# Kernel optimization log

Measured on AMD Instinct MI355X. Metric: run time of the kernel, lower is better.

The kernel has to match this reference:

```python
import jax, jax.numpy as jnp
import numpy as np
import math

D_MODEL = 1024
N_HEADS = 16
D_K = D_MODEL // N_HEADS
SEQ_LEN = 2048
BATCH = 2


def setup_inputs() -> dict:
    key = jax.random.key(0)
    ks = jax.random.split(key, 5)
    X = jax.random.normal(ks[0], (BATCH, SEQ_LEN, D_MODEL), dtype=jnp.float32)
    # Linear params (torch Linear: y = x @ W.T + b). Store as [in, out] for einsum.
    sc1 = 1.0 / math.sqrt(D_MODEL)
    W_qkv = jax.random.uniform(ks[1], (D_MODEL, 3 * D_MODEL), jnp.float32, -sc1, sc1)
    b_qkv = jax.random.uniform(ks[2], (3 * D_MODEL,), jnp.float32, -sc1, sc1)
    W_out = jax.random.uniform(ks[3], (D_MODEL, D_MODEL), jnp.float32, -sc1, sc1)
    b_out = jax.random.uniform(ks[4], (D_MODEL,), jnp.float32, -sc1, sc1)
    return {"X": X, "W_qkv": W_qkv, "b_qkv": b_qkv, "W_out": W_out, "b_out": b_out}


def reference(X, W_qkv, b_qkv, W_out, b_out):
    B, S, E = X.shape
    qkv = X @ W_qkv + b_qkv                       # [B,S,3E]
    qkv = qkv.reshape(B, S, 3, N_HEADS, D_K)
    q = jnp.transpose(qkv[:, :, 0], (0, 2, 1, 3))  # [B,H,S,Dk]
    k = jnp.transpose(qkv[:, :, 1], (0, 2, 1, 3))
    v = jnp.transpose(qkv[:, :, 2], (0, 2, 1, 3))
    scores = jnp.einsum('bhqd,bhkd->bhqk', q, k) / math.sqrt(D_K)
    causal = jnp.tril(jnp.ones((S, S), dtype=bool))
    scores = jnp.where(causal[None, None], scores, -jnp.inf)
    probs = jax.nn.softmax(scores, axis=-1)
    out = jnp.einsum('bhqk,bhkd->bhqd', probs, v)  # [B,H,S,Dk]
    out = jnp.transpose(out, (0, 2, 1, 3)).reshape(B, S, E)
    return out @ W_out + b_out
```

## Files before the change

### kernel.cpp

```cpp
#include <hip/hip_runtime.h>

typedef __bf16 bf16_t;
typedef bf16_t bf16x8 __attribute__((ext_vector_type(8)));
typedef bf16_t bf16x4 __attribute__((ext_vector_type(4)));
typedef float f32x4 __attribute__((ext_vector_type(4)));

#define SEQLEN 2048
#define EMB 1024
#define NHEADS 16
#define N3 3072
#define NBATCH 2
#define NEG_INF (-__builtin_inff())
#define SC2 0.18033688011112042f

__device__ __forceinline__ void async16(bf16_t* lds, const bf16_t* g) {
    __builtin_amdgcn_global_load_lds(
        (const __attribute__((address_space(1))) void*)g,
        (__attribute__((address_space(3))) void*)lds, 16, 0, 0);
}

__global__ __launch_bounds__(256) void transpose_weights(
    const float* __restrict__ Wqkv, const float* __restrict__ Wout,
    bf16_t* __restrict__ Wqkv_t, bf16_t* __restrict__ Wout_t)
{
    __shared__ float tile[64][65];
    int bx = blockIdx.x;
    const int k0 = blockIdx.y * 64;
    const float* W; bf16_t* Wt; int N; float s;
    if (bx < 48) { W = Wqkv; Wt = Wqkv_t; N = N3;  s = (bx * 64 < EMB) ? SC2 : 1.0f; }
    else         { bx -= 48; W = Wout; Wt = Wout_t; N = EMB; s = 1.0f; }
    const int n0 = bx * 64;
    const int t = threadIdx.x;
    const int nl = t & 63, k4 = t >> 6;
#pragma unroll
    for (int i = 0; i < 16; ++i) {
        int kk = k4 + i * 4;
        tile[kk][nl] = W[(size_t)(k0 + kk) * N + n0 + nl];
    }
    __syncthreads();
    const int kl = t & 63, n4 = t >> 6;
#pragma unroll
    for (int i = 0; i < 16; ++i) {
        int nn = n4 + i * 4;
        Wt[(size_t)(n0 + nn) * EMB + k0 + kl] = (bf16_t)(tile[kl][nn] * s);
    }
}

__global__ __launch_bounds__(256) void cvt_f32_bf16(
    const float* __restrict__ in, bf16_t* __restrict__ out, int n)
{
    const int i = (blockIdx.x * 256 + threadIdx.x) * 8;
    if (i >= n) return;
    float4 a = *(const float4*)&in[i];
    float4 b = *(const float4*)&in[i + 4];
    bf16_t v[8];
    v[0] = (bf16_t)a.x; v[1] = (bf16_t)a.y; v[2] = (bf16_t)a.z; v[3] = (bf16_t)a.w;
    v[4] = (bf16_t)b.x; v[5] = (bf16_t)b.y; v[6] = (bf16_t)b.z; v[7] = (bf16_t)b.w;
    *(float4*)&out[i] = *(float4*)&v[0];
}

template<bool OUT_BF16, bool V_SPLIT>
__global__ __launch_bounds__(256) void gemm_bt_kernel(
    const bf16_t* __restrict__ A, const bf16_t* __restrict__ Bt,
    const float* __restrict__ bias, void* __restrict__ Cp,
    bf16_t* __restrict__ vt, int scale_q,
    int Mdim, int Ndim, int Kdim)
{
    __shared__ bf16_t As[128 * 64];
    __shared__ bf16_t Bs[128 * 64];
    const int nb = Ndim >> 7;
    const int cpx = gridDim.x >> 3;
    const int bid = (blockIdx.x & 7) * cpx + (blockIdx.x >> 3);
    const int bx = bid % nb, by = bid / nb;
    const int r0 = by << 7, c0 = bx << 7;
    const int t = threadIdx.x, lane = t & 63;
    const int wid = t >> 6;
    const int wm = wid >> 1, wn = wid & 1;
    const int lr = lane & 15, lg = lane >> 4;

    const int glrow = wid * 32 + (lane >> 3);
    const int gsw = ((lane & 7) ^ (lane >> 3)) << 3;
    const bf16_t* gA = &A[(size_t)(r0 + glrow) * Kdim + gsw];
    const bf16_t* gB = &Bt[(size_t)(c0 + glrow) * Kdim + gsw];
    bf16_t* ldsA = &As[wid * 2048];
    bf16_t* ldsB = &Bs[wid * 2048];
    const size_t row8 = (size_t)8 * Kdim;

    const int fragb0 = (lr * 128 + lg * 16) ^ ((lr & 7) << 4);
    const int fragb1 = (lr * 128 + 64 + lg * 16) ^ ((lr & 7) << 4);

    f32x4 acc[4][4] = {};
    const int KT = Kdim >> 6;
    for (int kt = 0; kt < KT; ++kt) {
        const bf16_t* a = gA + kt * 64;
        const bf16_t* b = gB + kt * 64;
        async16(ldsA,        a);
        async16(ldsA + 512,  a + row8);
        async16(ldsA + 1024, a + 2 * row8);
        async16(ldsA + 1536, a + 3 * row8);
        async16(ldsB,        b);
        async16(ldsB + 512,  b + row8);
        async16(ldsB + 1024, b + 2 * row8);
        async16(ldsB + 1536, b + 3 * row8);
        __syncthreads();

        const char* Ab = (const char*)As + wm * 8192;
        const char* Bb = (const char*)Bs + wn * 8192;
        bf16x8 af[4], bfm[4];
#pragma unroll
        for (int m = 0; m < 4; ++m)
            af[m] = *(const bf16x8*)(Ab + m * 2048 + fragb0);
#pragma unroll
        for (int n = 0; n < 4; ++n)
            bfm[n] = *(const bf16x8*)(Bb + n * 2048 + fragb0);
#pragma unroll
        for (int m = 0; m < 4; ++m)
#pragma unroll
            for (int n = 0; n < 4; ++n)
                acc[m][n] = __builtin_amdgcn_mfma_f32_16x16x32_bf16(
                    af[m], bfm[n], acc[m][n], 0, 0, 0);
#pragma unroll
        for (int m = 0; m < 4; ++m)
            af[m] = *(const bf16x8*)(Ab + m * 2048 + fragb1);
#pragma unroll
        for (int n = 0; n < 4; ++n)
            bfm[n] = *(const bf16x8*)(Bb + n * 2048 + fragb1);
#pragma unroll
        for (int m = 0; m < 4; ++m)
#pragma unroll
            for (int n = 0; n < 4; ++n)
                acc[m][n] = __builtin_amdgcn_mfma_f32_16x16x32_bf16(
                    af[m], bfm[n], acc[m][n], 0, 0, 0);
        __syncthreads();
    }

    const bool vmode = V_SPLIT && (c0 >= 2 * EMB);
#pragma unroll
    for (int m = 0; m < 4; ++m) {
#pragma unroll
        for (int n = 0; n < 4; ++n) {
            const int col = c0 + wn * 64 + n * 16 + lr;
            float bval = bias[col];
            if (scale_q && col < EMB) bval *= SC2;
            if (vmode) {
                const int h = (col - 2 * EMB) >> 6, dd = col & 63;
                const int bb = r0 >> 11;
                const int sbase = (r0 & (SEQLEN - 1)) + wm * 64 + m * 16 + lg * 4;
                bf16x4 pk;
#pragma unroll
                for (int j = 0; j < 4; ++j) pk[j] = (bf16_t)(acc[m][n][j] + bval);
                *(bf16x4*)&vt[(size_t)((bb * 16 + h) * 64 + dd) * SEQLEN + sbase] = pk;
            } else {
#pragma unroll
                for (int j = 0; j < 4; ++j) {
                    const int row = r0 + wm * 64 + m * 16 + lg * 4 + j;
                    const float v = acc[m][n][j] + bval;
                    if (OUT_BF16)
                        ((bf16_t*)Cp)[(size_t)row * Ndim + col] = (bf16_t)v;
                    else
                        ((float*)Cp)[(size_t)row * Ndim + col] = v;
                }
            }
        }
    }
}

__global__ __launch_bounds__(256, 4) void attn_kernel(
    const bf16_t* __restrict__ qkv, const bf16_t* __restrict__ vt,
    bf16_t* __restrict__ attn_out)
{
    __shared__ bf16_t Kl[2][4096];
    __shared__ bf16_t Vl[2][4096];
    const int d = blockIdx.x;
    const int r = d >> 8;
    const int u = (d >> 3) & 31;
    int qt = (r & 1) ? (31 - u) : u;
    if (r & 2) qt ^= 16;
    const int bh = (d & 7) + (r << 3);
    const int b = bh >> 4, h = bh & 15;
    const int q0 = qt << 6;
    const int t = threadIdx.x, lane = t & 63, wid = t >> 6;
    const int lr = lane & 15, lg = lane >> 4;
    const int sr = t >> 2, sc16 = (t & 3) << 4;

    const int fragb0 = (lr * 128 + lg * 16) ^ ((lr & 7) << 4);
    const int fragb1 = (lr * 128 + 64 + lg * 16) ^ ((lr & 7) << 4);
    const int stb0   = (sr * 128 + sc16 * 2) ^ ((sr & 7) << 4);
    const int stb1   = (sr * 128 + sc16 * 2 + 16) ^ ((sr & 7) << 4);

    const bf16_t* kp = &qkv[(size_t)(b * SEQLEN + sr) * N3 + EMB + h * 64 + sc16];
    const bf16_t* vp = &vt[(size_t)(bh * 64 + sr) * SEQLEN + sc16];
    const size_t kstep = (size_t)64 * N3;

    const int qg = q0 + wid * 16 + lr;
    bf16x8 qa0, qa1;
    {
        const bf16_t* qb = &qkv[(size_t)(b * SEQLEN + qg) * N3 + h * 64];
        qa0 = *(const bf16x8*)&qb[lg * 8];
        qa1 = *(const bf16x8*)&qb[32 + lg * 8];
    }
    bf16x8 ones;
#pragma unroll
    for (int i = 0; i < 8; ++i) ones[i] = (bf16_t)1.0f;

    f32x4 o[4] = {};
    f32x4 ol = {};
    float m_run = NEG_INF;

    auto stK = [&](char* base, float4 a, float4 c) {
        *(float4*)(base + stb0) = a; *(float4*)(base + stb1) = c;
    };
    auto stV = [&](char* base, float4 a, float4 c) {
        float4 w0 = {a.x, a.y, c.x, c.y};
        float4 w1 = {a.z, a.w, c.z, c.w};
        *(float4*)(base + stb0) = w0; *(float4*)(base + stb1) = w1;
    };

    {
        float4 k0 = *(const float4*)kp, k1 = *(const float4*)(kp + 8);
        float4 v0 = *(const float4*)vp, v1 = *(const float4*)(vp + 8);
        stK((char*)Kl[0], k0, k1);
        stV((char*)Vl[0], v0, v1);
    }
    __syncthreads();
    int cur = 0;
    for (int kt = 0; kt <= qt; ++kt) {
        float4 nk0, nk1, nv0, nv1;
        const bool more = (kt < qt);
        if (more) {
            kp += kstep; vp += 64;
            nk0 = *(const float4*)kp; nk1 = *(const float4*)(kp + 8);
            nv0 = *(const float4*)vp; nv1 = *(const float4*)(vp + 8);
        }

        const char* Kc = (const char*)Kl[cur];
        const char* Vc = (const char*)Vl[cur];

        f32x4 sc[4] = {};
        __builtin_amdgcn_s_setprio(1);
#pragma unroll
        for (int n = 0; n < 4; ++n) {
            bf16x8 kb0 = *(const bf16x8*)(Kc + (fragb0 + n * 2048));
            bf16x8 kb1 = *(const bf16x8*)(Kc + (fragb1 + n * 2048));
            sc[n] = __builtin_amdgcn_mfma_f32_16x16x32_bf16(kb0, qa0, sc[n], 0, 0, 0);
            sc[n] = __builtin_amdgcn_mfma_f32_16x16x32_bf16(kb1, qa1, sc[n], 0, 0, 0);
        }
        __builtin_amdgcn_s_setprio(0);

        if (kt == qt) {
#pragma unroll
            for (int n = 0; n < 4; ++n)
#pragma unroll
                for (int j = 0; j < 4; ++j) {
                    const int kg = kt * 64 + n * 16 + lg * 4 + j;
                    sc[n][j] = (kg <= qg) ? sc[n][j] : NEG_INF;
                }
        }
        float mx[4];
#pragma unroll
        for (int n = 0; n < 4; ++n)
            mx[n] = fmaxf(fmaxf(fmaxf(sc[n][0], sc[n][1]), sc[n][2]), sc[n][3]);
        float pmax = fmaxf(fmaxf(fmaxf(mx[0], mx[1]), mx[2]), mx[3]);

        if (__any(pmax > m_run + 8.f)) {
            float pm = fmaxf(pmax, __shfl_xor(pmax, 16));
            pm = fmaxf(pm, __shfl_xor(pm, 32));
            const float mnew = fmaxf(m_run, pm);
            const float alpha = exp2f(m_run - mnew);
            m_run = mnew;
            float al[4];
#pragma unroll
            for (int j = 0; j < 4; ++j) al[j] = __shfl(alpha, lg * 4 + j);
#pragma unroll
            for (int dn = 0; dn < 4; ++dn)
#pragma unroll
                for (int j = 0; j < 4; ++j) o[dn][j] *= al[j];
#pragma unroll
            for (int j = 0; j < 4; ++j) ol[j] *= al[j];
        }

#pragma unroll
        for (int n = 0; n < 4; ++n)
#pragma unroll
            for (int j = 0; j < 4; ++j) sc[n][j] = exp2f(sc[n][j] - m_run);

        unsigned pk00, pk01, pk10, pk11, pk20, pk21, pk30, pk31;
        asm("v_cvt_pk_bf16_f32 %0, %1, %2" : "=v"(pk00) : "v"(sc[0][0]), "v"(sc[0][1]));
        asm("v_cvt_pk_bf16_f32 %0, %1, %2" : "=v"(pk01) : "v"(sc[0][2]), "v"(sc[0][3]));
        asm("v_cvt_pk_bf16_f32 %0, %1, %2" : "=v"(pk10) : "v"(sc[1][0]), "v"(sc[1][1]));
        asm("v_cvt_pk_bf16_f32 %0, %1, %2" : "=v"(pk11) : "v"(sc[1][2]), "v"(sc[1][3]));
        asm("v_cvt_pk_bf16_f32 %0, %1, %2" : "=v"(pk20) : "v"(sc[2][0]), "v"(sc[2][1]));
        asm("v_cvt_pk_bf16_f32 %0, %1, %2" : "=v"(pk21) : "v"(sc[2][2]), "v"(sc[2][3]));
        asm("v_cvt_pk_bf16_f32 %0, %1, %2" : "=v"(pk30) : "v"(sc[3][0]), "v"(sc[3][1]));
        asm("v_cvt_pk_bf16_f32 %0, %1, %2" : "=v"(pk31) : "v"(sc[3][2]), "v"(sc[3][3]));
        asm("v_permlane32_swap_b32 %0, %1" : "+v"(pk00), "+v"(pk10));
        asm("v_permlane32_swap_b32 %0, %1" : "+v"(pk01), "+v"(pk11));
        asm("v_permlane32_swap_b32 %0, %1" : "+v"(pk20), "+v"(pk30));
        asm("v_permlane32_swap_b32 %0, %1" : "+v"(pk21), "+v"(pk31));
        union UW { unsigned w[4]; bf16x8 v; };
        UW ua, ub;
        ua.w[0] = pk00; ua.w[1] = pk01; ua.w[2] = pk10; ua.w[3] = pk11;
        ub.w[0] = pk20; ub.w[1] = pk21; ub.w[2] = pk30; ub.w[3] = pk31;
        const bf16x8 pa0 = ua.v, pa1 = ub.v;

        __builtin_amdgcn_s_setprio(1);
#pragma unroll
        for (int dn = 0; dn < 4; ++dn) {
            bf16x8 vb0 = *(const bf16x8*)(Vc + (fragb0 + dn * 2048));
            bf16x8 vb1 = *(const bf16x8*)(Vc + (fragb1 + dn * 2048));
            o[dn] = __builtin_amdgcn_mfma_f32_16x16x32_bf16(pa0, vb0, o[dn], 0, 0, 0);
            o[dn] = __builtin_amdgcn_mfma_f32_16x16x32_bf16(pa1, vb1, o[dn], 0, 0, 0);
        }
        ol = __builtin_amdgcn_mfma_f32_16x16x32_bf16(pa0, ones, ol, 0, 0, 0);
        ol = __builtin_amdgcn_mfma_f32_16x16x32_bf16(pa1, ones, ol, 0, 0, 0);
        __builtin_amdgcn_s_setprio(0);

        if (more) {
            stK((char*)Kl[cur ^ 1], nk0, nk1);
            stV((char*)Vl[cur ^ 1], nv0, nv1);
        }
        __syncthreads();
        cur ^= 1;
    }

    float li[4];
#pragma unroll
    for (int j = 0; j < 4; ++j) li[j] = 1.0f / ol[j];
#pragma unroll
    for (int dn = 0; dn < 4; ++dn)
#pragma unroll
        for (int j = 0; j < 4; ++j) {
            const int row = b * SEQLEN + q0 + wid * 16 + lg * 4 + j;
            attn_out[(size_t)row * EMB + h * 64 + dn * 16 + lr] =
                (bf16_t)(o[dn][j] * li[j]);
        }
}

extern "C" void kernel_launch(void* const* d_in, const int* in_sizes, int n_in,
                              void* d_out, int out_size, void* d_ws, size_t ws_size,
                              hipStream_t stream)
{
    const float* X     = (const float*)d_in[0];
    const float* W_qkv = (const float*)d_in[1];
    const float* b_qkv = (const float*)d_in[2];
    const float* W_out = (const float*)d_in[3];
    const float* b_out = (const float*)d_in[4];
    float* out = (float*)d_out;

    char* ws = (char*)d_ws;
    bf16_t* Wqkv_t = (bf16_t*)ws;
    bf16_t* Wout_t = (bf16_t*)(ws + 6u * 1024 * 1024);
    bf16_t* qkv    = (bf16_t*)(ws + 8u * 1024 * 1024);
    bf16_t* attn   = (bf16_t*)(ws + 32u * 1024 * 1024);
    bf16_t* Xb     = (bf16_t*)(ws + 40u * 1024 * 1024);
    bf16_t* Vt_g   = (bf16_t*)(ws + 48u * 1024 * 1024);

    dim3 blk(256);
    transpose_weights<<<dim3(64, 16), blk, 0, stream>>>(W_qkv, W_out, Wqkv_t, Wout_t);
    cvt_f32_bf16<<<4096 * 1024 / (256 * 8), blk, 0, stream>>>(X, Xb, 4096 * 1024);

    gemm_bt_kernel<true, true><<<(4096 / 128) * (N3 / 128), blk, 0, stream>>>(
        Xb, Wqkv_t, b_qkv, (void*)qkv, Vt_g, 1, 4096, N3, EMB);

    attn_kernel<<<32 * 32, blk, 0, stream>>>(qkv, Vt_g, attn);

    gemm_bt_kernel<false, false><<<(4096 / 128) * (EMB / 128), blk, 0, stream>>>(
        attn, Wout_t, b_out, (void*)out, nullptr, 0, 4096, EMB, EMB);
}
```

Measured before the change: 110.9 us.

## Double attention query tile to 128 rows per block, sharing K/V tiles

Each attention block now handles 128 query rows (two 16-row sub-tiles per wave) instead of 64, so every K/V tile loaded into LDS feeds twice as many MFMAs. The grid halves to 512 blocks, uses a new pairing of complementary causal tiles across two rounds, and launch bounds drop to 2 blocks per CU to make room for the extra registers. The aim is to cut global/LDS K/V traffic per unit of work and raise MFMA density. The cost is fewer blocks, lower occupancy and coarser causal load balance, with some wasted masked work on the diagonal tiles.

```diff
diff --git a/kernel.cpp b/kernel.cpp
--- a/kernel.cpp
+++ b/kernel.cpp
@@ -165,7 +165,7 @@
     }
 }
 
-__global__ __launch_bounds__(256, 4) void attn_kernel(
+__global__ __launch_bounds__(256, 2) void attn_kernel(
     const bf16_t* __restrict__ qkv, const bf16_t* __restrict__ vt,
     bf16_t* __restrict__ attn_out)
 {
@@ -173,12 +173,13 @@
     __shared__ bf16_t Vl[2][4096];
     const int d = blockIdx.x;
     const int r = d >> 8;
-    const int u = (d >> 3) & 31;
-    int qt = (r & 1) ? (31 - u) : u;
-    if (r & 2) qt ^= 16;
-    const int bh = (d & 7) + (r << 3);
+    const int idx = d & 255;
+    const int bh = idx & 31;
+    const int u = idx >> 5;
+    const int qt = r ? (15 - u) : u;
     const int b = bh >> 4, h = bh & 15;
-    const int q0 = qt << 6;
+    const int q0 = qt << 7;
+    const int ktend = 2 * qt + 1;
     const int t = threadIdx.x, lane = t & 63, wid = t >> 6;
     const int lr = lane & 15, lg = lane >> 4;
     const int sr = t >> 2, sc16 = (t & 3) << 4;
@@ -192,20 +193,25 @@
     const bf16_t* vp = &vt[(size_t)(bh * 64 + sr) * SEQLEN + sc16];
     const size_t kstep = (size_t)64 * N3;
 
-    const int qg = q0 + wid * 16 + lr;
-    bf16x8 qa0, qa1;
+    const int qb0 = q0 + wid * 32;
+    const int qb1 = qb0 + 16;
+    const int qg0 = qb0 + lr, qg1 = qb1 + lr;
+    bf16x8 qa0, qa1, qa2, qa3;
     {
-        const bf16_t* qb = &qkv[(size_t)(b * SEQLEN + qg) * N3 + h * 64];
-        qa0 = *(const bf16x8*)&qb[lg * 8];
-        qa1 = *(const bf16x8*)&qb[32 + lg * 8];
+        const bf16_t* q0p = &qkv[(size_t)(b * SEQLEN + qg0) * N3 + h * 64];
+        const bf16_t* q1p = &qkv[(size_t)(b * SEQLEN + qg1) * N3 + h * 64];
+        qa0 = *(const bf16x8*)&q0p[lg * 8];
+        qa1 = *(const bf16x8*)&q0p[32 + lg * 8];
+        qa2 = *(const bf16x8*)&q1p[lg * 8];
+        qa3 = *(const bf16x8*)&q1p[32 + lg * 8];
     }
     bf16x8 ones;
 #pragma unroll
     for (int i = 0; i < 8; ++i) ones[i] = (bf16_t)1.0f;
 
-    f32x4 o[4] = {};
-    f32x4 ol = {};
-    float m_run = NEG_INF;
+    f32x4 o0[4] = {}, o1[4] = {};
+    f32x4 ol0 = {}, ol1 = {};
+    float m0 = NEG_INF, m1 = NEG_INF;
 
     auto stK = [&](char* base, float4 a, float4 c) {
         *(float4*)(base + stb0) = a; *(float4*)(base + stb1) = c;
@@ -224,9 +230,9 @@
     }
     __syncthreads();
     int cur = 0;
-    for (int kt = 0; kt <= qt; ++kt) {
+    for (int kt = 0; kt <= ktend; ++kt) {
         float4 nk0, nk1, nv0, nv1;
-        const bool more = (kt < qt);
+        const bool more = (kt < ktend);
         if (more) {
             kp += kstep; vp += 64;
             nk0 = *(const float4*)kp; nk1 = *(const float4*)(kp + 8);
@@ -236,83 +242,136 @@
         const char* Kc = (const char*)Kl[cur];
         const char* Vc = (const char*)Vl[cur];
 
-        f32x4 sc[4] = {};
+        f32x4 s0[4] = {}, s1[4] = {};
         __builtin_amdgcn_s_setprio(1);
 #pragma unroll
         for (int n = 0; n < 4; ++n) {
             bf16x8 kb0 = *(const bf16x8*)(Kc + (fragb0 + n * 2048));
             bf16x8 kb1 = *(const bf16x8*)(Kc + (fragb1 + n * 2048));
-            sc[n] = __builtin_amdgcn_mfma_f32_16x16x32_bf16(kb0, qa0, sc[n], 0, 0, 0);
-            sc[n] = __builtin_amdgcn_mfma_f32_16x16x32_bf16(kb1, qa1, sc[n], 0, 0, 0);
+            s0[n] = __builtin_amdgcn_mfma_f32_16x16x32_bf16(kb0, qa0, s0[n], 0, 0, 0);
+            s0[n] = __builtin_amdgcn_mfma_f32_16x16x32_bf16(kb1, qa1, s0[n], 0, 0, 0);
+            s1[n] = __builtin_amdgcn_mfma_f32_16x16x32_bf16(kb0, qa2, s1[n], 0, 0, 0);
+            s1[n] = __builtin_amdgcn_mfma_f32_16x16x32_bf16(kb1, qa3, s1[n], 0, 0, 0);
         }
         __builtin_amdgcn_s_setprio(0);
 
-        if (kt == qt) {
+        const int kbase = kt << 6;
+        if (kbase + 63 > qb0) {
 #pragma unroll
             for (int n = 0; n < 4; ++n)
 #pragma unroll
                 for (int j = 0; j < 4; ++j) {
-                    const int kg = kt * 64 + n * 16 + lg * 4 + j;
-                    sc[n][j] = (kg <= qg) ? sc[n][j] : NEG_INF;
+                    const int kg = kbase + n * 16 + lg * 4 + j;
+                    s0[n][j] = (kg <= qg0) ? s0[n][j] : NEG_INF;
                 }
         }
-        float mx[4];
+        if (kbase + 63 > qb1) {
+#pragma unroll
+            for (int n = 0; n < 4; ++n)
+#pragma unroll
+                for (int j = 0; j < 4; ++j) {
+                    const int kg = kbase + n * 16 + lg * 4 + j;
+                    s1[n][j] = (kg <= qg1) ? s1[n][j] : NEG_INF;
+                }
+        }
+
+        float pm0 = NEG_INF, pm1 = NEG_INF;
+#pragma unroll
+        for (int n = 0; n < 4; ++n) {
+            pm0 = fmaxf(pm0, fmaxf(fmaxf(s0[n][0], s0[n][1]), fmaxf(s0[n][2], s0[n][3])));
+            pm1 = fmaxf(pm1, fmaxf(fmaxf(s1[n][0], s1[n][1]), fmaxf(s1[n][2], s1[n][3])));
+        }
+
+        if (__any((pm0 > m0 + 8.f) || (pm1 > m1 + 8.f))) {
+            float pa = fmaxf(pm0, __shfl_xor(pm0, 16));
+            pa = fmaxf(pa, __shfl_xor(pa, 32));
+            float pb = fmaxf(pm1, __shfl_xor(pm1, 16));
+            pb = fmaxf(pb, __shfl_xor(pb, 32));
+            const float mn0 = fmaxf(m0, pa);
+            const float mn1 = fmaxf(m1, pb);
+            const float a0 = exp2f(m0 - mn0);
+            const float a1 = exp2f(m1 - mn1);
+            m0 = mn0; m1 = mn1;
+            float al0[4], al1[4];
+#pragma unroll
+            for (int j = 0; j < 4; ++j) {
+                al0[j] = __shfl(a0, lg * 4 + j);
+                al1[j] = __shfl(a1, lg * 4 + j);
+            }
+#pragma unroll
+            for (int dn = 0; dn < 4; ++dn)
+#pragma unroll
+                for (int j = 0; j < 4; ++j) {
+                    o0[dn][j] *= al0[j];
+                    o1[dn][j] *= al1[j];
+                }
+#pragma unroll
+            for (int j = 0; j < 4; ++j) { ol0[j] *= al0[j]; ol1[j] *= al1[j]; }
+        }
+
 #pragma unroll
         for (int n = 0; n < 4; ++n)
-            mx[n] = fmaxf(fmaxf(fmaxf(sc[n][0], sc[n][1]), sc[n][2]), sc[n][3]);
-        float pmax = fmaxf(fmaxf(fmaxf(mx[0], mx[1]), mx[2]), mx[3]);
-
-        if (__any(pmax > m_run + 8.f)) {
-            float pm = fmaxf(pmax, __shfl_xor(pmax, 16));
-            pm = fmaxf(pm, __shfl_xor(pm, 32));
-            const float mnew = fmaxf(m_run, pm);
-            const float alpha = exp2f(m_run - mnew);
-            m_run = mnew;
-            float al[4];
-#pragma unroll
-            for (int j = 0; j < 4; ++j) al[j] = __shfl(alpha, lg * 4 + j);
-#pragma unroll
-            for (int dn = 0; dn < 4; ++dn)
-#pragma unroll
-                for (int j = 0; j < 4; ++j) o[dn][j] *= al[j];
-#pragma unroll
-            for (int j = 0; j < 4; ++j) ol[j] *= al[j];
-        }
-
-#pragma unroll
-        for (int n = 0; n < 4; ++n)
-#pragma unroll
-            for (int j = 0; j < 4; ++j) sc[n][j] = exp2f(sc[n][j] - m_run);
-
-        unsigned pk00, pk01, pk10, pk11, pk20, pk21, pk30, pk31;
-        asm("v_cvt_pk_bf16_f32 %0, %1, %2" : "=v"(pk00) : "v"(sc[0][0]), "v"(sc[0][1]));
-        asm("v_cvt_pk_bf16_f32 %0, %1, %2" : "=v"(pk01) : "v"(sc[0][2]), "v"(sc[0][3]));
-        asm("v_cvt_pk_bf16_f32 %0, %1, %2" : "=v"(pk10) : "v"(sc[1][0]), "v"(sc[1][1]));
-        asm("v_cvt_pk_bf16_f32 %0, %1, %2" : "=v"(pk11) : "v"(sc[1][2]), "v"(sc[1][3]));
-        asm("v_cvt_pk_bf16_f32 %0, %1, %2" : "=v"(pk20) : "v"(sc[2][0]), "v"(sc[2][1]));
-        asm("v_cvt_pk_bf16_f32 %0, %1, %2" : "=v"(pk21) : "v"(sc[2][2]), "v"(sc[2][3]));
-        asm("v_cvt_pk_bf16_f32 %0, %1, %2" : "=v"(pk30) : "v"(sc[3][0]), "v"(sc[3][1]));
-        asm("v_cvt_pk_bf16_f32 %0, %1, %2" : "=v"(pk31) : "v"(sc[3][2]), "v"(sc[3][3]));
-        asm("v_permlane32_swap_b32 %0, %1" : "+v"(pk00), "+v"(pk10));
-        asm("v_permlane32_swap_b32 %0, %1" : "+v"(pk01), "+v"(pk11));
-        asm("v_permlane32_swap_b32 %0, %1" : "+v"(pk20), "+v"(pk30));
-        asm("v_permlane32_swap_b32 %0, %1" : "+v"(pk21), "+v"(pk31));
+#pragma unroll
+            for (int j = 0; j < 4; ++j) {
+                s0[n][j] = exp2f(s0[n][j] - m0);
+                s1[n][j] = exp2f(s1[n][j] - m1);
+            }
+
         union UW { unsigned w[4]; bf16x8 v; };
-        UW ua, ub;
-        ua.w[0] = pk00; ua.w[1] = pk01; ua.w[2] = pk10; ua.w[3] = pk11;
-        ub.w[0] = pk20; ub.w[1] = pk21; ub.w[2] = pk30; ub.w[3] = pk31;
-        const bf16x8 pa0 = ua.v, pa1 = ub.v;
+        bf16x8 pa0s0, pa1s0, pa0s1, pa1s1;
+        {
+            unsigned pk00, pk01, pk10, pk11, pk20, pk21, pk30, pk31;
+            asm("v_cvt_pk_bf16_f32 %0, %1, %2" : "=v"(pk00) : "v"(s0[0][0]), "v"(s0[0][1]));
+            asm("v_cvt_pk_bf16_f32 %0, %1, %2" : "=v"(pk01) : "v"(s0[0][2]), "v"(s0[0][3]));
+            asm("v_cvt_pk_bf16_f32 %0, %1, %2" : "=v"(pk10) : "v"(s0[1][0]), "v"(s0[1][1]));
+            asm("v_cvt_pk_bf16_f32 %0, %1, %2" : "=v"(pk11) : "v"(s0[1][2]), "v"(s0[1][3]));
+            asm("v_cvt_pk_bf16_f32 %0, %1, %2" : "=v"(pk20) : "v"(s0[2][0]), "v"(s0[2][1]));
+            asm("v_cvt_pk_bf16_f32 %0, %1, %2" : "=v"(pk21) : "v"(s0[2][2]), "v"(s0[2][3]));
+            asm("v_cvt_pk_bf16_f32 %0, %1, %2" : "=v"(pk30) : "v"(s0[3][0]), "v"(s0[3][1]));
+            asm("v_cvt_pk_bf16_f32 %0, %1, %2" : "=v"(pk31) : "v"(s0[3][2]), "v"(s0[3][3]));
+            asm("v_permlane32_swap_b32 %0, %1" : "+v"(pk00), "+v"(pk10));
+            asm("v_permlane32_swap_b32 %0, %1" : "+v"(pk01), "+v"(pk11));
+            asm("v_permlane32_swap_b32 %0, %1" : "+v"(pk20), "+v"(pk30));
+            asm("v_permlane32_swap_b32 %0, %1" : "+v"(pk21), "+v"(pk31));
+            UW ua, ub;
+            ua.w[0] = pk00; ua.w[1] = pk01; ua.w[2] = pk10; ua.w[3] = pk11;
+            ub.w[0] = pk20; ub.w[1] = pk21; ub.w[2] = pk30; ub.w[3] = pk31;
+            pa0s0 = ua.v; pa1s0 = ub.v;
+        }
+        {
+            unsigned pk00, pk01, pk10, pk11, pk20, pk21, pk30, pk31;
+            asm("v_cvt_pk_bf16_f32 %0, %1, %2" : "=v"(pk00) : "v"(s1[0][0]), "v"(s1[0][1]));
+            asm("v_cvt_pk_bf16_f32 %0, %1, %2" : "=v"(pk01) : "v"(s1[0][2]), "v"(s1[0][3]));
+            asm("v_cvt_pk_bf16_f32 %0, %1, %2" : "=v"(pk10) : "v"(s1[1][0]), "v"(s1[1][1]));
+            asm("v_cvt_pk_bf16_f32 %0, %1, %2" : "=v"(pk11) : "v"(s1[1][2]), "v"(s1[1][3]));
+            asm("v_cvt_pk_bf16_f32 %0, %1, %2" : "=v"(pk20) : "v"(s1[2][0]), "v"(s1[2][1]));
+            asm("v_cvt_pk_bf16_f32 %0, %1, %2" : "=v"(pk21) : "v"(s1[2][2]), "v"(s1[2][3]));
+            asm("v_cvt_pk_bf16_f32 %0, %1, %2" : "=v"(pk30) : "v"(s1[3][0]), "v"(s1[3][1]));
+            asm("v_cvt_pk_bf16_f32 %0, %1, %2" : "=v"(pk31) : "v"(s1[3][2]), "v"(s1[3][3]));
+            asm("v_permlane32_swap_b32 %0, %1" : "+v"(pk00), "+v"(pk10));
+            asm("v_permlane32_swap_b32 %0, %1" : "+v"(pk01), "+v"(pk11));
+            asm("v_permlane32_swap_b32 %0, %1" : "+v"(pk20), "+v"(pk30));
+            asm("v_permlane32_swap_b32 %0, %1" : "+v"(pk21), "+v"(pk31));
+            UW ua, ub;
+            ua.w[0] = pk00; ua.w[1] = pk01; ua.w[2] = pk10; ua.w[3] = pk11;
+            ub.w[0] = pk20; ub.w[1] = pk21; ub.w[2] = pk30; ub.w[3] = pk31;
+            pa0s1 = ua.v; pa1s1 = ub.v;
+        }
 
         __builtin_amdgcn_s_setprio(1);
 #pragma unroll
         for (int dn = 0; dn < 4; ++dn) {
             bf16x8 vb0 = *(const bf16x8*)(Vc + (fragb0 + dn * 2048));
             bf16x8 vb1 = *(const bf16x8*)(Vc + (fragb1 + dn * 2048));
-            o[dn] = __builtin_amdgcn_mfma_f32_16x16x32_bf16(pa0, vb0, o[dn], 0, 0, 0);
-            o[dn] = __builtin_amdgcn_mfma_f32_16x16x32_bf16(pa1, vb1, o[dn], 0, 0, 0);
-        }
-        ol = __builtin_amdgcn_mfma_f32_16x16x32_bf16(pa0, ones, ol, 0, 0, 0);
-        ol = __builtin_amdgcn_mfma_f32_16x16x32_bf16(pa1, ones, ol, 0, 0, 0);
+            o0[dn] = __builtin_amdgcn_mfma_f32_16x16x32_bf16(pa0s0, vb0, o0[dn], 0, 0, 0);
+            o0[dn] = __builtin_amdgcn_mfma_f32_16x16x32_bf16(pa1s0, vb1, o0[dn], 0, 0, 0);
+            o1[dn] = __builtin_amdgcn_mfma_f32_16x16x32_bf16(pa0s1, vb0, o1[dn], 0, 0, 0);
+            o1[dn] = __builtin_amdgcn_mfma_f32_16x16x32_bf16(pa1s1, vb1, o1[dn], 0, 0, 0);
+        }
+        ol0 = __builtin_amdgcn_mfma_f32_16x16x32_bf16(pa0s0, ones, ol0, 0, 0, 0);
+        ol0 = __builtin_amdgcn_mfma_f32_16x16x32_bf16(pa1s0, ones, ol0, 0, 0, 0);
+        ol1 = __builtin_amdgcn_mfma_f32_16x16x32_bf16(pa0s1, ones, ol1, 0, 0, 0);
+        ol1 = __builtin_amdgcn_mfma_f32_16x16x32_bf16(pa1s1, ones, ol1, 0, 0, 0);
         __builtin_amdgcn_s_setprio(0);
 
         if (more) {
@@ -323,16 +382,18 @@
         cur ^= 1;
     }
 
-    float li[4];
-#pragma unroll
-    for (int j = 0; j < 4; ++j) li[j] = 1.0f / ol[j];
+    float li0[4], li1[4];
+#pragma unroll
+    for (int j = 0; j < 4; ++j) { li0[j] = 1.0f / ol0[j]; li1[j] = 1.0f / ol1[j]; }
 #pragma unroll
     for (int dn = 0; dn < 4; ++dn)
 #pragma unroll
         for (int j = 0; j < 4; ++j) {
-            const int row = b * SEQLEN + q0 + wid * 16 + lg * 4 + j;
-            attn_out[(size_t)row * EMB + h * 64 + dn * 16 + lr] =
-                (bf16_t)(o[dn][j] * li[j]);
+            const int row0 = b * SEQLEN + qb0 + lg * 4 + j;
+            const int row1 = b * SEQLEN + qb1 + lg * 4 + j;
+            const int col = h * 64 + dn * 16 + lr;
+            attn_out[(size_t)row0 * EMB + col] = (bf16_t)(o0[dn][j] * li0[j]);
+            attn_out[(size_t)row1 * EMB + col] = (bf16_t)(o1[dn][j] * li1[j]);
         }
 }
 
@@ -362,7 +423,7 @@
     gemm_bt_kernel<true, true><<<(4096 / 128) * (N3 / 128), blk, 0, stream>>>(
         Xb, Wqkv_t, b_qkv, (void*)qkv, Vt_g, 1, 4096, N3, EMB);
 
-    attn_kernel<<<32 * 32, blk, 0, stream>>>(qkv, Vt_g, attn);
+    attn_kernel<<<512, blk, 0, stream>>>(qkv, Vt_g, attn);
 
     gemm_bt_kernel<false, false><<<(4096 / 128) * (EMB / 128), blk, 0, stream>>>(
         attn, Wout_t, b_out, (void*)out, nullptr, 0, 4096, EMB, EMB);
```

Measured after the change: 113.7 us. 1.03x slower.

## Use async global-to-LDS loads in attention and fuse prep kernels

Applied to the files above, without the earlier changes.

The attention kernel now stages K and V tiles with global_load_lds async copies straight into LDS instead of going through registers. It relies on a swizzled source addressing, and a permuted V^T store order in the QKV GEMM epilogue makes the LDS layout match the fragment reads. The weight transpose and X conversion kernels are merged into one launch to cut launch overhead. The gain is fewer registers and VALU stores in the attention loop. The risks are a correctness dependence on the new layout permutation and async completion ordering relative to __syncthreads.

```diff
diff --git a/kernel.cpp b/kernel.cpp
--- a/kernel.cpp
+++ b/kernel.cpp
@@ -19,18 +19,31 @@
         (__attribute__((address_space(3))) void*)lds, 16, 0, 0);
 }
 
-__global__ __launch_bounds__(256) void transpose_weights(
-    const float* __restrict__ Wqkv, const float* __restrict__ Wout,
+__global__ __launch_bounds__(256) void prep_kernel(
+    const float* __restrict__ X, const float* __restrict__ Wqkv,
+    const float* __restrict__ Wout, bf16_t* __restrict__ Xb,
     bf16_t* __restrict__ Wqkv_t, bf16_t* __restrict__ Wout_t)
 {
     __shared__ float tile[64][65];
-    int bx = blockIdx.x;
-    const int k0 = blockIdx.y * 64;
+    const int id = blockIdx.x;
+    const int t = threadIdx.x;
+    if (id < 2048) {
+        const int i = (id * 256 + t) * 8;
+        float4 a = *(const float4*)&X[i];
+        float4 b = *(const float4*)&X[i + 4];
+        bf16_t v[8];
+        v[0] = (bf16_t)a.x; v[1] = (bf16_t)a.y; v[2] = (bf16_t)a.z; v[3] = (bf16_t)a.w;
+        v[4] = (bf16_t)b.x; v[5] = (bf16_t)b.y; v[6] = (bf16_t)b.z; v[7] = (bf16_t)b.w;
+        *(float4*)&Xb[i] = *(float4*)&v[0];
+        return;
+    }
+    const int wid2 = id - 2048;
+    int bx = wid2 & 63;
+    const int k0 = (wid2 >> 6) << 6;
     const float* W; bf16_t* Wt; int N; float s;
     if (bx < 48) { W = Wqkv; Wt = Wqkv_t; N = N3;  s = (bx * 64 < EMB) ? SC2 : 1.0f; }
     else         { bx -= 48; W = Wout; Wt = Wout_t; N = EMB; s = 1.0f; }
     const int n0 = bx * 64;
-    const int t = threadIdx.x;
     const int nl = t & 63, k4 = t >> 6;
 #pragma unroll
     for (int i = 0; i < 16; ++i) {
@@ -44,19 +57,6 @@
         int nn = n4 + i * 4;
         Wt[(size_t)(n0 + nn) * EMB + k0 + kl] = (bf16_t)(tile[kl][nn] * s);
     }
-}
-
-__global__ __launch_bounds__(256) void cvt_f32_bf16(
-    const float* __restrict__ in, bf16_t* __restrict__ out, int n)
-{
-    const int i = (blockIdx.x * 256 + threadIdx.x) * 8;
-    if (i >= n) return;
-    float4 a = *(const float4*)&in[i];
-    float4 b = *(const float4*)&in[i + 4];
-    bf16_t v[8];
-    v[0] = (bf16_t)a.x; v[1] = (bf16_t)a.y; v[2] = (bf16_t)a.z; v[3] = (bf16_t)a.w;
-    v[4] = (bf16_t)b.x; v[5] = (bf16_t)b.y; v[6] = (bf16_t)b.z; v[7] = (bf16_t)b.w;
-    *(float4*)&out[i] = *(float4*)&v[0];
 }
 
 template<bool OUT_BF16, bool V_SPLIT>
@@ -135,6 +135,7 @@
     }
 
     const bool vmode = V_SPLIT && (c0 >= 2 * EMB);
+    const int lgp = ((lg & 1) << 1) | (lg >> 1);
 #pragma unroll
     for (int m = 0; m < 4; ++m) {
 #pragma unroll
@@ -145,7 +146,7 @@
             if (vmode) {
                 const int h = (col - 2 * EMB) >> 6, dd = col & 63;
                 const int bb = r0 >> 11;
-                const int sbase = (r0 & (SEQLEN - 1)) + wm * 64 + m * 16 + lg * 4;
+                const int sbase = (r0 & (SEQLEN - 1)) + wm * 64 + m * 16 + lgp * 4;
                 bf16x4 pk;
 #pragma unroll
                 for (int j = 0; j < 4; ++j) pk[j] = (bf16_t)(acc[m][n][j] + bval);
@@ -181,16 +182,26 @@
     const int q0 = qt << 6;
     const int t = threadIdx.x, lane = t & 63, wid = t >> 6;
     const int lr = lane & 15, lg = lane >> 4;
-    const int sr = t >> 2, sc16 = (t & 3) << 4;
 
     const int fragb0 = (lr * 128 + lg * 16) ^ ((lr & 7) << 4);
     const int fragb1 = (lr * 128 + 64 + lg * 16) ^ ((lr & 7) << 4);
-    const int stb0   = (sr * 128 + sc16 * 2) ^ ((sr & 7) << 4);
-    const int stb1   = (sr * 128 + sc16 * 2 + 16) ^ ((sr & 7) << 4);
-
-    const bf16_t* kp = &qkv[(size_t)(b * SEQLEN + sr) * N3 + EMB + h * 64 + sc16];
-    const bf16_t* vp = &vt[(size_t)(bh * 64 + sr) * SEQLEN + sc16];
-    const size_t kstep = (size_t)64 * N3;
+
+    const int srow = wid * 8 + (lane >> 3);
+    const int ssw  = ((lane & 7) ^ (lane >> 3)) << 3;
+    const bf16_t* kp = &qkv[(size_t)(b * SEQLEN + srow) * N3 + EMB + h * 64 + ssw];
+    const bf16_t* vp = &vt[(size_t)(bh * 64 + srow) * SEQLEN + ssw];
+    const size_t kstep  = (size_t)64 * N3;
+    const size_t krow32 = (size_t)32 * N3;
+    const size_t vrow32 = (size_t)32 * SEQLEN;
+
+    auto stage = [&](int buf) {
+        bf16_t* k0 = &Kl[buf][wid * 512];
+        bf16_t* v0 = &Vl[buf][wid * 512];
+        async16(k0,        kp);
+        async16(k0 + 2048, kp + krow32);
+        async16(v0,        vp);
+        async16(v0 + 2048, vp + vrow32);
+    };
 
     const int qg = q0 + wid * 16 + lr;
     bf16x8 qa0, qa1;
@@ -207,30 +218,14 @@
     f32x4 ol = {};
     float m_run = NEG_INF;
 
-    auto stK = [&](char* base, float4 a, float4 c) {
-        *(float4*)(base + stb0) = a; *(float4*)(base + stb1) = c;
-    };
-    auto stV = [&](char* base, float4 a, float4 c) {
-        float4 w0 = {a.x, a.y, c.x, c.y};
-        float4 w1 = {a.z, a.w, c.z, c.w};
-        *(float4*)(base + stb0) = w0; *(float4*)(base + stb1) = w1;
-    };
-
-    {
-        float4 k0 = *(const float4*)kp, k1 = *(const float4*)(kp + 8);
-        float4 v0 = *(const float4*)vp, v1 = *(const float4*)(vp + 8);
-        stK((char*)Kl[0], k0, k1);
-        stV((char*)Vl[0], v0, v1);
-    }
+    stage(0);
     __syncthreads();
     int cur = 0;
     for (int kt = 0; kt <= qt; ++kt) {
-        float4 nk0, nk1, nv0, nv1;
         const bool more = (kt < qt);
         if (more) {
             kp += kstep; vp += 64;
-            nk0 = *(const float4*)kp; nk1 = *(const float4*)(kp + 8);
-            nv0 = *(const float4*)vp; nv1 = *(const float4*)(vp + 8);
+            stage(cur ^ 1);
         }
 
         const char* Kc = (const char*)Kl[cur];
@@ -315,10 +310,6 @@
         ol = __builtin_amdgcn_mfma_f32_16x16x32_bf16(pa1, ones, ol, 0, 0, 0);
         __builtin_amdgcn_s_setprio(0);
 
-        if (more) {
-            stK((char*)Kl[cur ^ 1], nk0, nk1);
-            stV((char*)Vl[cur ^ 1], nv0, nv1);
-        }
         __syncthreads();
         cur ^= 1;
     }
@@ -356,8 +347,7 @@
     bf16_t* Vt_g   = (bf16_t*)(ws + 48u * 1024 * 1024);
 
     dim3 blk(256);
-    transpose_weights<<<dim3(64, 16), blk, 0, stream>>>(W_qkv, W_out, Wqkv_t, Wout_t);
-    cvt_f32_bf16<<<4096 * 1024 / (256 * 8), blk, 0, stream>>>(X, Xb, 4096 * 1024);
+    prep_kernel<<<3072, blk, 0, stream>>>(X, W_qkv, W_out, Xb, Wqkv_t, Wout_t);
 
     gemm_bt_kernel<true, true><<<(4096 / 128) * (N3 / 128), blk, 0, stream>>>(
         Xb, Wqkv_t, b_qkv, (void*)qkv, Vt_g, 1, 4096, N3, EMB);
```

New measurement: 114.8 us. +3.5%, slower.
